# Optimization experiments

Hardware: AMD Instinct MI355X
Metric: run time of the kernel (lower is better)

The kernel has to match this reference:

```python
import jax, jax.numpy as jnp
import numpy as np

D_MODEL = 1024
NUM_HEADS = 16
D_HEAD = D_MODEL // NUM_HEADS


def setup_inputs() -> dict:
    key = jax.random.key(0)
    k1, k2, k3, k4, k5 = jax.random.split(key, 5)
    B, S = 2, 2048
    x = jax.random.normal(k1, (B, S, D_MODEL), dtype=jnp.float32)
    mask = jnp.ones((B, S), dtype=bool)
    # nn.Linear default init: U(-1/sqrt(fan_in), 1/sqrt(fan_in))
    lim = 1.0 / np.sqrt(D_MODEL)
    W_qkv = jax.random.uniform(k2, (D_MODEL, 3 * D_MODEL), jnp.float32, -lim, lim)
    b_qkv = jax.random.uniform(k3, (3 * D_MODEL,), jnp.float32, -lim, lim)
    W_out = jax.random.uniform(k4, (D_MODEL, D_MODEL), jnp.float32, -lim, lim)
    b_out = jax.random.uniform(k5, (D_MODEL,), jnp.float32, -lim, lim)
    return {"x": x, "mask": mask, "W_qkv": W_qkv, "b_qkv": b_qkv,
            "W_out": W_out, "b_out": b_out}


def reference(x, mask, W_qkv, b_qkv, W_out, b_out):
    B, S, _ = x.shape
    qkv = x @ W_qkv + b_qkv  # [B,S,3*D]
    q, k, v = jnp.split(qkv, 3, axis=-1)
    # [B,S,D] -> [B,H,S,dh]
    def heads(t):
        return t.reshape(B, S, NUM_HEADS, D_HEAD).transpose(0, 2, 1, 3)
    q, k, v = heads(q), heads(k), heads(v)
    scores = jnp.einsum('bhqd,bhkd->bhqk', q, k) / np.sqrt(D_HEAD).astype(np.float32)
    # 2-D mask -> broadcast over heads and query positions (key padding mask)
    scores = jnp.where(mask[:, None, None, :], scores, -jnp.inf)
    attn = jax.nn.softmax(scores, axis=-1)
    out = jnp.einsum('bhqk,bhkd->bhqd', attn, v)
    out = out.transpose(0, 2, 1, 3).reshape(B, S, D_MODEL)
    return out @ W_out + b_out
```

## Files before the change

kernel.cpp:

```cpp
#include <hip/hip_runtime.h>

typedef unsigned short u16;
typedef __bf16 bf16x8 __attribute__((ext_vector_type(8)));
typedef float f32x4 __attribute__((ext_vector_type(4)));


__device__ __forceinline__ u16 f2bf(float f) {
  union { float f; unsigned int u; } c; c.f = f;
  unsigned int u = c.u;
  u += 0x7fffu + ((u >> 16) & 1u);
  return (u16)(u >> 16);
}

__device__ __forceinline__ void async_copy16(const void* g, void* l) {
  __builtin_amdgcn_global_load_lds(
      (const __attribute__((address_space(1))) void*)g,
      (__attribute__((address_space(3))) void*)l, 16, 0, 0);
}

__global__ __launch_bounds__(256) void prep_kernel(const float4* __restrict__ x,
                                                   ushort4* __restrict__ xb,
                                                   const float* __restrict__ Wqkv,
                                                   u16* __restrict__ WqkvT,
                                                   const float* __restrict__ Wout,
                                                   u16* __restrict__ WoutT) {
  __shared__ float tile[64][65];
  int blk = blockIdx.x, tid = threadIdx.x;
  if (blk < 4096) {
    int i = blk * 256 + tid;
    float4 v = x[i];
    ushort4 r;
    r.x = f2bf(v.x); r.y = f2bf(v.y); r.z = f2bf(v.z); r.w = f2bf(v.w);
    xb[i] = r;
    return;
  }
  const float* W; u16* WT; int K = 1024, N, n0, k0;
  if (blk < 4864) {
    int b2 = blk - 4096; N = 3072; n0 = (b2 % 48) * 64; k0 = (b2 / 48) * 64;
    W = Wqkv; WT = WqkvT;
  } else {
    int b2 = blk - 4864; N = 1024; n0 = (b2 % 16) * 64; k0 = (b2 / 16) * 64;
    W = Wout; WT = WoutT;
  }
#pragma unroll
  for (int p = 0; p < 16; ++p) {
    int idx = tid + p * 256;
    int r = idx >> 6, c = idx & 63;
    tile[r][c] = W[(size_t)(k0 + r) * N + n0 + c];
  }
  __syncthreads();
#pragma unroll
  for (int p = 0; p < 16; ++p) {
    int idx = tid + p * 256;
    int ro = idx >> 6, co = idx & 63;
    WT[(size_t)(n0 + ro) * K + k0 + co] = f2bf(tile[co][ro]);
  }
}

template <int NT>
__global__ __launch_bounds__(256, 3)
void gemm_bt_kernel(const u16* __restrict__ A, const u16* __restrict__ Bt,
                    const float* __restrict__ bias, int mode,
                    u16* __restrict__ qp, u16* __restrict__ kp, u16* __restrict__ vp,
                    float* __restrict__ outp) {
  constexpr int NI = NT / 32;
  constexpr int BCOPIES = NT / 32;
  __shared__ __align__(16) u16 As[128 * 64];
  __shared__ __align__(16) u16 Bs[NT * 64];
  int tid = threadIdx.x;
  int w = tid >> 6, lane = tid & 63, quad = lane >> 4, lr = lane & 15;
  int wm = w & 1, wn = w >> 1;
  int n0 = blockIdx.x * NT, m0 = blockIdx.y * 128;
  const char* Ab = (const char*)A;
  const char* Bb = (const char*)Bt;

  size_t aoff[4], boff[BCOPIES];
  int ldsb[4];
#pragma unroll
  for (int i = 0; i < 4; ++i) {
    int slot = i * 256 + tid;
    int row = slot >> 3, g = (slot & 7) ^ (row & 7);
    aoff[i] = (size_t)(m0 + row) * 2048 + g * 16;
    ldsb[i] = (i * 256 + w * 64) * 16;
  }
#pragma unroll
  for (int i = 0; i < BCOPIES; ++i) {
    int slot = i * 256 + tid;
    int row = slot >> 3, g = (slot & 7) ^ (row & 7);
    boff[i] = (size_t)(n0 + row) * 2048 + g * 16;
  }

  f32x4 acc[4][NI];
#pragma unroll
  for (int i = 0; i < 4; ++i)
#pragma unroll
    for (int j = 0; j < NI; ++j) { f32x4 z = {0.f, 0.f, 0.f, 0.f}; acc[i][j] = z; }

  for (int kt = 0; kt < 16; ++kt) {
    __syncthreads();
#pragma unroll
    for (int i = 0; i < 4; ++i)
      async_copy16(Ab + aoff[i] + kt * 128, (char*)As + ldsb[i]);
#pragma unroll
    for (int i = 0; i < BCOPIES; ++i)
      async_copy16(Bb + boff[i] + kt * 128, (char*)Bs + ldsb[i]);
    __syncthreads();

    bf16x8 af[4][2], bfr[NI][2];
#pragma unroll
    for (int mi = 0; mi < 4; ++mi) {
      int row = wm * 64 + mi * 16 + lr;
#pragma unroll
      for (int kc = 0; kc < 2; ++kc)
        af[mi][kc] = *(const bf16x8*)((const char*)As + row * 128 +
                                      (((kc * 4 + quad) ^ (row & 7)) * 16));
    }
#pragma unroll
    for (int ni = 0; ni < NI; ++ni) {
      int row = wn * (NT / 2) + ni * 16 + lr;
#pragma unroll
      for (int kc = 0; kc < 2; ++kc)
        bfr[ni][kc] = *(const bf16x8*)((const char*)Bs + row * 128 +
                                       (((kc * 4 + quad) ^ (row & 7)) * 16));
    }
#pragma unroll
    for (int mi = 0; mi < 4; ++mi)
#pragma unroll
      for (int ni = 0; ni < NI; ++ni) {
        acc[mi][ni] = __builtin_amdgcn_mfma_f32_16x16x32_bf16(af[mi][0], bfr[ni][0], acc[mi][ni], 0, 0, 0);
        acc[mi][ni] = __builtin_amdgcn_mfma_f32_16x16x32_bf16(af[mi][1], bfr[ni][1], acc[mi][ni], 0, 0, 0);
      }
  }

  const float QSCALE = 0.125f * 1.4426950408889634f;
#pragma unroll
  for (int mi = 0; mi < 4; ++mi)
#pragma unroll
    for (int ni = 0; ni < NI; ++ni)
#pragma unroll
      for (int r = 0; r < 4; ++r) {
        int row = m0 + wm * 64 + mi * 16 + quad * 4 + r;
        int col = n0 + wn * (NT / 2) + ni * 16 + lr;
        float val = acc[mi][ni][r] + bias[col];
        if (mode == 0) {
          int t = col >> 10, c = col & 1023, h = c >> 6, d = c & 63;
          int b = row >> 11, s = row & 2047;
          int bh = b * 16 + h;
          if (t == 0)      qp[(((size_t)bh * 2048 + s) << 6) + d] = f2bf(val * QSCALE);
          else if (t == 1) kp[(((size_t)bh * 2048 + s) << 6) + d] = f2bf(val);
          else             vp[((size_t)bh * 64 + d) * 2048 + s] = f2bf(val);
        } else {
          outp[(size_t)row * 1024 + col] = val;
        }
      }
}

__global__ __launch_bounds__(256, 2)
void attn_kernel(const u16* __restrict__ q, const u16* __restrict__ k,
                 const u16* __restrict__ vT, u16* __restrict__ aout) {
  __shared__ __align__(16) u16 Ks[2][8192];
  __shared__ __align__(16) u16 Vs[2][8192];
  int tid = threadIdx.x;
  int w = tid >> 6, lane = tid & 63, quad = lane >> 4, lr = lane & 15;
  int blk = blockIdx.x;
  int j = blk >> 3;
  int bh = (blk & 7) * 4 + (j >> 4), qt = j & 15;
  int b = bh >> 4, h = bh & 15;
  const u16* qp = q + (size_t)bh * 2048 * 64;
  const char* kB = (const char*)(k + (size_t)bh * 2048 * 64);
  const char* vB = (const char*)(vT + (size_t)bh * 64 * 2048);
  int q0 = qt * 128 + w * 32;

  bf16x8 qf[2][2];
#pragma unroll
  for (int qg = 0; qg < 2; ++qg)
#pragma unroll
    for (int kc = 0; kc < 2; ++kc)
      qf[qg][kc] = *(const bf16x8*)&qp[(size_t)(q0 + qg * 16 + lr) * 64 + kc * 32 + quad * 8];

  bf16x8 ones;
  {
    union { bf16x8 v; u16 e[8]; } t;
#pragma unroll
    for (int i = 0; i < 8; ++i) t.e[i] = 0x3F80;
    ones = t.v;
  }

  f32x4 o[2][4];
  f32x4 lacc[2];
#pragma unroll
  for (int qg = 0; qg < 2; ++qg) {
    f32x4 z = {0.f, 0.f, 0.f, 0.f};
    lacc[qg] = z;
#pragma unroll
    for (int mi = 0; mi < 4; ++mi) o[qg][mi] = z;
  }

  size_t koff[4], voff[4];
  int ldsb[4];
#pragma unroll
  for (int c = 0; c < 4; ++c) {
    int slot = (c * 4 + w) * 64 + lane;
    int krow = slot >> 3, kch = slot & 7;
    int kg = kch ^ (krow & 7);
    int r5 = krow & 31;
    int gk = (krow & 96) + ((r5 & 15) >> 2) * 8 + ((r5 >> 4) & 1) * 4 + (r5 & 3);
    koff[c] = (size_t)gk * 128 + kg * 16;
    int vrow = slot >> 4, vch = slot & 15;
    int vg = vch ^ (vrow & 15);
    voff[c] = (size_t)vrow * 4096 + vg * 16;
    ldsb[c] = (c * 4 + w) * 1024;
  }

#pragma unroll
  for (int c = 0; c < 4; ++c) {
    async_copy16(kB + koff[c], (char*)Ks[0] + ldsb[c]);
    async_copy16(vB + voff[c], (char*)Vs[0] + ldsb[c]);
  }
  __syncthreads();

  for (int kt2 = 0; kt2 < 8; ++kt2) {
#pragma unroll
    for (int sub = 0; sub < 2; ++sub) {
      int kt = kt2 * 2 + sub;
      if (kt < 15) {
        int nxt = sub ^ 1;
#pragma unroll
        for (int c = 0; c < 4; ++c) {
          async_copy16(kB + (size_t)(kt + 1) * 16384 + koff[c], (char*)Ks[nxt] + ldsb[c]);
          async_copy16(vB + (size_t)(kt + 1) * 256 + voff[c], (char*)Vs[nxt] + ldsb[c]);
        }
      }

#pragma unroll
      for (int kg = 0; kg < 4; ++kg) {
        bf16x8 kf[2][2];
#pragma unroll
        for (int half = 0; half < 2; ++half) {
          int row = kg * 32 + half * 16 + lr;
#pragma unroll
          for (int kc = 0; kc < 2; ++kc)
            kf[half][kc] = *(const bf16x8*)((const char*)Ks[sub] + row * 128 +
                                            (((kc * 4 + quad) ^ (row & 7)) * 16));
        }
        bf16x8 vf[4];
#pragma unroll
        for (int mi = 0; mi < 4; ++mi) {
          int d = mi * 16 + lr;
          vf[mi] = *(const bf16x8*)((const char*)Vs[sub] + d * 256 +
                                    (((kg * 4 + quad) ^ (d & 15)) * 16));
        }

#pragma unroll
        for (int qg = 0; qg < 2; ++qg) {
          f32x4 St[2];
#pragma unroll
          for (int half = 0; half < 2; ++half) {
            f32x4 z = {0.f, 0.f, 0.f, 0.f};
            St[half] = __builtin_amdgcn_mfma_f32_16x16x32_bf16(kf[half][0], qf[qg][0], z, 0, 0, 0);
            St[half] = __builtin_amdgcn_mfma_f32_16x16x32_bf16(kf[half][1], qf[qg][1], St[half], 0, 0, 0);
          }
          union { bf16x8 v; unsigned int u[4]; } pu;
#pragma unroll
          for (int half = 0; half < 2; ++half)
#pragma unroll
            for (int pr = 0; pr < 2; ++pr) {
              union { float f; unsigned int u; } a, bb;
              a.f  = exp2f(St[half][pr * 2 + 0]);
              bb.f = exp2f(St[half][pr * 2 + 1]);
              pu.u[half * 2 + pr] =
                  __builtin_amdgcn_perm(bb.u + 0x8000u, a.u + 0x8000u, 0x07060302u);
            }
          lacc[qg] = __builtin_amdgcn_mfma_f32_16x16x32_bf16(pu.v, ones, lacc[qg], 0, 0, 0);
#pragma unroll
          for (int mi = 0; mi < 4; ++mi)
            o[qg][mi] = __builtin_amdgcn_mfma_f32_16x16x32_bf16(pu.v, vf[mi], o[qg][mi], 0, 0, 0);
        }
      }

      __syncthreads();
    }
  }

#pragma unroll
  for (int qg = 0; qg < 2; ++qg) {
    float linv[4];
#pragma unroll
    for (int r = 0; r < 4; ++r) linv[r] = 1.0f / lacc[qg][r];
#pragma unroll
    for (int mi = 0; mi < 4; ++mi)
#pragma unroll
      for (int r = 0; r < 4; ++r) {
        int srow = q0 + qg * 16 + quad * 4 + r;
        int d = mi * 16 + lr;
        aout[(size_t)(b * 2048 + srow) * 1024 + h * 64 + d] = f2bf(o[qg][mi][r] * linv[r]);
      }
  }
}

extern "C" void kernel_launch(void* const* d_in, const int* in_sizes, int n_in,
                              void* d_out, int out_size, void* d_ws, size_t ws_size,
                              hipStream_t stream) {
  const float* x    = (const float*)d_in[0];
  const float* Wqkv = (const float*)d_in[2];
  const float* bqkv = (const float*)d_in[3];
  const float* Wout = (const float*)d_in[4];
  const float* bout = (const float*)d_in[5];
  float* out = (float*)d_out;

  char* ws = (char*)d_ws;
  u16* xb    = (u16*)(ws);
  u16* WqkvT = (u16*)(ws + (size_t)(8  << 20));
  u16* WoutT = (u16*)(ws + (size_t)(14 << 20));
  u16* qb    = (u16*)(ws + (size_t)(16 << 20));
  u16* kb    = (u16*)(ws + (size_t)(24 << 20));
  u16* vTb   = (u16*)(ws + (size_t)(32 << 20));
  u16* aob   = xb;

  prep_kernel<<<5120, 256, 0, stream>>>((const float4*)x, (ushort4*)xb,
                                        Wqkv, WqkvT, Wout, WoutT);
  gemm_bt_kernel<128><<<dim3(24, 32), 256, 0, stream>>>(xb, WqkvT, bqkv, 0, qb, kb, vTb, nullptr);
  attn_kernel<<<512, 256, 0, stream>>>(qb, kb, vTb, aob);
  gemm_bt_kernel<64><<<dim3(16, 32), 256, 0, stream>>>(aob, WoutT, bout, 1, nullptr, nullptr, nullptr, out);
}
```

Measured before the change: 198.3 us.

## Halve attention tile sizes to double blocks and raise occupancy

Each attention block now handles 64 queries (16 per wave) and streams keys in 64-row tiles instead of 128, halving LDS buffers and per-thread accumulators. The grid doubles to 1024 blocks and launch bounds ask for 4 blocks per CU, to improve latency hiding and spread work more evenly across CUs. In exchange, each K/V tile loaded into LDS is reused by fewer queries, so global and LDS traffic per FLOP rises and there are twice as many barriers per block.

```diff
diff --git a/kernel.cpp b/kernel.cpp
--- a/kernel.cpp
+++ b/kernel.cpp
@@ -155,28 +155,25 @@
       }
 }
 
-__global__ __launch_bounds__(256, 2)
+__global__ __launch_bounds__(256, 4)
 void attn_kernel(const u16* __restrict__ q, const u16* __restrict__ k,
                  const u16* __restrict__ vT, u16* __restrict__ aout) {
-  __shared__ __align__(16) u16 Ks[2][8192];
-  __shared__ __align__(16) u16 Vs[2][8192];
+  __shared__ __align__(16) u16 Ks[2][4096];
+  __shared__ __align__(16) u16 Vs[2][4096];
   int tid = threadIdx.x;
   int w = tid >> 6, lane = tid & 63, quad = lane >> 4, lr = lane & 15;
   int blk = blockIdx.x;
-  int j = blk >> 3;
-  int bh = (blk & 7) * 4 + (j >> 4), qt = j & 15;
+  int bh = (blk & 7) * 4 + (blk >> 8), qt = (blk >> 3) & 31;
   int b = bh >> 4, h = bh & 15;
   const u16* qp = q + (size_t)bh * 2048 * 64;
   const char* kB = (const char*)(k + (size_t)bh * 2048 * 64);
   const char* vB = (const char*)(vT + (size_t)bh * 64 * 2048);
-  int q0 = qt * 128 + w * 32;
-
-  bf16x8 qf[2][2];
-#pragma unroll
-  for (int qg = 0; qg < 2; ++qg)
-#pragma unroll
-    for (int kc = 0; kc < 2; ++kc)
-      qf[qg][kc] = *(const bf16x8*)&qp[(size_t)(q0 + qg * 16 + lr) * 64 + kc * 32 + quad * 8];
+  int q0 = qt * 64 + w * 16;
+
+  bf16x8 qf[2];
+#pragma unroll
+  for (int kc = 0; kc < 2; ++kc)
+    qf[kc] = *(const bf16x8*)&qp[(size_t)(q0 + lr) * 64 + kc * 32 + quad * 8];
 
   bf16x8 ones;
   {
@@ -186,54 +183,53 @@
     ones = t.v;
   }
 
-  f32x4 o[2][4];
-  f32x4 lacc[2];
-#pragma unroll
-  for (int qg = 0; qg < 2; ++qg) {
+  f32x4 o[4];
+  f32x4 lacc;
+  {
     f32x4 z = {0.f, 0.f, 0.f, 0.f};
-    lacc[qg] = z;
-#pragma unroll
-    for (int mi = 0; mi < 4; ++mi) o[qg][mi] = z;
-  }
-
-  size_t koff[4], voff[4];
-  int ldsb[4];
-#pragma unroll
-  for (int c = 0; c < 4; ++c) {
+    lacc = z;
+#pragma unroll
+    for (int mi = 0; mi < 4; ++mi) o[mi] = z;
+  }
+
+  size_t koff[2], voff[2];
+  int ldsb[2];
+#pragma unroll
+  for (int c = 0; c < 2; ++c) {
     int slot = (c * 4 + w) * 64 + lane;
     int krow = slot >> 3, kch = slot & 7;
     int kg = kch ^ (krow & 7);
     int r5 = krow & 31;
-    int gk = (krow & 96) + ((r5 & 15) >> 2) * 8 + ((r5 >> 4) & 1) * 4 + (r5 & 3);
+    int gk = (krow & 32) + ((r5 & 15) >> 2) * 8 + ((r5 >> 4) & 1) * 4 + (r5 & 3);
     koff[c] = (size_t)gk * 128 + kg * 16;
-    int vrow = slot >> 4, vch = slot & 15;
-    int vg = vch ^ (vrow & 15);
+    int vrow = slot >> 3, vch = slot & 7;
+    int vg = vch ^ (vrow & 7);
     voff[c] = (size_t)vrow * 4096 + vg * 16;
     ldsb[c] = (c * 4 + w) * 1024;
   }
 
 #pragma unroll
-  for (int c = 0; c < 4; ++c) {
+  for (int c = 0; c < 2; ++c) {
     async_copy16(kB + koff[c], (char*)Ks[0] + ldsb[c]);
     async_copy16(vB + voff[c], (char*)Vs[0] + ldsb[c]);
   }
   __syncthreads();
 
-  for (int kt2 = 0; kt2 < 8; ++kt2) {
+  for (int kt2 = 0; kt2 < 16; ++kt2) {
 #pragma unroll
     for (int sub = 0; sub < 2; ++sub) {
       int kt = kt2 * 2 + sub;
-      if (kt < 15) {
+      if (kt < 31) {
         int nxt = sub ^ 1;
 #pragma unroll
-        for (int c = 0; c < 4; ++c) {
-          async_copy16(kB + (size_t)(kt + 1) * 16384 + koff[c], (char*)Ks[nxt] + ldsb[c]);
-          async_copy16(vB + (size_t)(kt + 1) * 256 + voff[c], (char*)Vs[nxt] + ldsb[c]);
+        for (int c = 0; c < 2; ++c) {
+          async_copy16(kB + (size_t)(kt + 1) * 8192 + koff[c], (char*)Ks[nxt] + ldsb[c]);
+          async_copy16(vB + (size_t)(kt + 1) * 128 + voff[c], (char*)Vs[nxt] + ldsb[c]);
         }
       }
 
 #pragma unroll
-      for (int kg = 0; kg < 4; ++kg) {
+      for (int kg = 0; kg < 2; ++kg) {
         bf16x8 kf[2][2];
 #pragma unroll
         for (int half = 0; half < 2; ++half) {
@@ -247,55 +243,49 @@
 #pragma unroll
         for (int mi = 0; mi < 4; ++mi) {
           int d = mi * 16 + lr;
-          vf[mi] = *(const bf16x8*)((const char*)Vs[sub] + d * 256 +
-                                    (((kg * 4 + quad) ^ (d & 15)) * 16));
-        }
-
-#pragma unroll
-        for (int qg = 0; qg < 2; ++qg) {
-          f32x4 St[2];
-#pragma unroll
-          for (int half = 0; half < 2; ++half) {
-            f32x4 z = {0.f, 0.f, 0.f, 0.f};
-            St[half] = __builtin_amdgcn_mfma_f32_16x16x32_bf16(kf[half][0], qf[qg][0], z, 0, 0, 0);
-            St[half] = __builtin_amdgcn_mfma_f32_16x16x32_bf16(kf[half][1], qf[qg][1], St[half], 0, 0, 0);
+          vf[mi] = *(const bf16x8*)((const char*)Vs[sub] + d * 128 +
+                                    (((kg * 4 + quad) ^ (d & 7)) * 16));
+        }
+
+        f32x4 St[2];
+#pragma unroll
+        for (int half = 0; half < 2; ++half) {
+          f32x4 z = {0.f, 0.f, 0.f, 0.f};
+          St[half] = __builtin_amdgcn_mfma_f32_16x16x32_bf16(kf[half][0], qf[0], z, 0, 0, 0);
+          St[half] = __builtin_amdgcn_mfma_f32_16x16x32_bf16(kf[half][1], qf[1], St[half], 0, 0, 0);
+        }
+        union { bf16x8 v; unsigned int u[4]; } pu;
+#pragma unroll
+        for (int half = 0; half < 2; ++half)
+#pragma unroll
+          for (int pr = 0; pr < 2; ++pr) {
+            union { float f; unsigned int u; } a, bb;
+            a.f  = exp2f(St[half][pr * 2 + 0]);
+            bb.f = exp2f(St[half][pr * 2 + 1]);
+            pu.u[half * 2 + pr] =
+                __builtin_amdgcn_perm(bb.u + 0x8000u, a.u + 0x8000u, 0x07060302u);
           }
-          union { bf16x8 v; unsigned int u[4]; } pu;
-#pragma unroll
-          for (int half = 0; half < 2; ++half)
-#pragma unroll
-            for (int pr = 0; pr < 2; ++pr) {
-              union { float f; unsigned int u; } a, bb;
-              a.f  = exp2f(St[half][pr * 2 + 0]);
-              bb.f = exp2f(St[half][pr * 2 + 1]);
-              pu.u[half * 2 + pr] =
-                  __builtin_amdgcn_perm(bb.u + 0x8000u, a.u + 0x8000u, 0x07060302u);
-            }
-          lacc[qg] = __builtin_amdgcn_mfma_f32_16x16x32_bf16(pu.v, ones, lacc[qg], 0, 0, 0);
-#pragma unroll
-          for (int mi = 0; mi < 4; ++mi)
-            o[qg][mi] = __builtin_amdgcn_mfma_f32_16x16x32_bf16(pu.v, vf[mi], o[qg][mi], 0, 0, 0);
-        }
+        lacc = __builtin_amdgcn_mfma_f32_16x16x32_bf16(pu.v, ones, lacc, 0, 0, 0);
+#pragma unroll
+        for (int mi = 0; mi < 4; ++mi)
+          o[mi] = __builtin_amdgcn_mfma_f32_16x16x32_bf16(pu.v, vf[mi], o[mi], 0, 0, 0);
       }
 
       __syncthreads();
     }
   }
 
-#pragma unroll
-  for (int qg = 0; qg < 2; ++qg) {
-    float linv[4];
-#pragma unroll
-    for (int r = 0; r < 4; ++r) linv[r] = 1.0f / lacc[qg][r];
-#pragma unroll
-    for (int mi = 0; mi < 4; ++mi)
-#pragma unroll
-      for (int r = 0; r < 4; ++r) {
-        int srow = q0 + qg * 16 + quad * 4 + r;
-        int d = mi * 16 + lr;
-        aout[(size_t)(b * 2048 + srow) * 1024 + h * 64 + d] = f2bf(o[qg][mi][r] * linv[r]);
-      }
-  }
+  float linv[4];
+#pragma unroll
+  for (int r = 0; r < 4; ++r) linv[r] = 1.0f / lacc[r];
+#pragma unroll
+  for (int mi = 0; mi < 4; ++mi)
+#pragma unroll
+    for (int r = 0; r < 4; ++r) {
+      int srow = q0 + quad * 4 + r;
+      int d = mi * 16 + lr;
+      aout[(size_t)(b * 2048 + srow) * 1024 + h * 64 + d] = f2bf(o[mi][r] * linv[r]);
+    }
 }
 
 extern "C" void kernel_launch(void* const* d_in, const int* in_sizes, int n_in,
@@ -320,6 +310,6 @@
   prep_kernel<<<5120, 256, 0, stream>>>((const float4*)x, (ushort4*)xb,
                                         Wqkv, WqkvT, Wout, WoutT);
   gemm_bt_kernel<128><<<dim3(24, 32), 256, 0, stream>>>(xb, WqkvT, bqkv, 0, qb, kb, vTb, nullptr);
-  attn_kernel<<<512, 256, 0, stream>>>(qb, kb, vTb, aob);
+  attn_kernel<<<1024, 256, 0, stream>>>(qb, kb, vTb, aob);
   gemm_bt_kernel<64><<<dim3(16, 32), 256, 0, stream>>>(aob, WoutT, bout, 1, nullptr, nullptr, nullptr, out);
 }
```

Result: no change. 197.3 us (-0.5%).
